# Kernel optimization log

Measured on AMD Instinct MI355X. Metric: run time of the kernel, lower is better.

Reference implementation:

```python
import jax, jax.numpy as jnp
import numpy as np

HID = 512
N_INT = 131072
N_INIT = 32768


def setup_inputs() -> dict:
    key = jax.random.key(0)
    ks = jax.random.split(key, 12)
    d = {}
    d["xt_int"] = jax.random.uniform(ks[0], (N_INT, 2), dtype=jnp.float32)
    d["f"] = 0.1 * jax.random.normal(ks[1], (N_INT, 1), dtype=jnp.float32)
    d["xt_init"] = jax.random.uniform(ks[2], (N_INIT, 2), dtype=jnp.float32)
    d["g"] = 0.1 * jax.random.normal(ks[3], (N_INIT, 1), dtype=jnp.float32)
    d["g_deriv"] = 0.1 * jax.random.normal(ks[4], (N_INIT, 1), dtype=jnp.float32)
    # tanh MLP 2 -> 512 -> 512 -> 512 -> 512 -> 1, Glorot-ish init
    def w(k, fi, fo):
        return jax.random.normal(k, (fi, fo), dtype=jnp.float32) * jnp.sqrt(2.0 / (fi + fo)).astype(jnp.float32)
    d["W0"] = w(ks[5], 2, HID);   d["b0"] = jnp.zeros((HID,), jnp.float32)
    d["W1"] = w(ks[6], HID, HID); d["b1"] = jnp.zeros((HID,), jnp.float32)
    d["W2"] = w(ks[7], HID, HID); d["b2"] = jnp.zeros((HID,), jnp.float32)
    d["W3"] = w(ks[8], HID, HID); d["b3"] = jnp.zeros((HID,), jnp.float32)
    d["W4"] = w(ks[9], HID, 1);   d["b4"] = jnp.zeros((1,), jnp.float32)
    d["c"] = jnp.ones((1,), jnp.float32)  # wave speed parameter
    return d


def _mlp(xt, Ws, bs):
    h = xt
    for W, b in zip(Ws[:-1], bs[:-1]):
        h = jnp.tanh(h @ W + b)
    return h @ Ws[-1] + bs[-1]  # [N, 1]


def reference(xt_int, f, xt_init, g, g_deriv, W0, b0, W1, b1, W2, b2, W3, b3, W4, b4, c):
    Ws = [W0, W1, W2, W3, W4]
    bs = [b0, b1, b2, b3, b4]
    net = lambda xt: _mlp(xt, Ws, bs)

    # --- initial-condition loss: 0.5/n * ||u(x,0) - g||^2
    n_init = xt_init.shape[0]
    pred_init = net(xt_init)
    loss_init = 0.5 / n_init * jnp.sum((pred_init - g) ** 2)

    # --- Neumann initial loss: u_t via forward-mode (tangent e_t = (0,1))
    e_t_init = jnp.broadcast_to(jnp.array([0.0, 1.0], jnp.float32), xt_init.shape)
    u_t_init = jax.jvp(net, (xt_init,), (e_t_init,))[1]
    loss_init_deriv = 0.5 / n_init * jnp.sum((u_t_init - g_deriv) ** 2)

    # --- PDE residual: u_tt - c^2 * u_xx via nested JVPs (batched, big GEMMs)
    n_int = xt_int.shape[0]

    def dir_deriv(v):
        # first directional derivative of net along constant direction v
        def d1(z):
            return jax.jvp(net, (z,), (jnp.broadcast_to(v, z.shape),))[1]
        return d1

    e_t = jnp.array([0.0, 1.0], jnp.float32)
    e_x = jnp.array([1.0, 0.0], jnp.float32)
    u_tt = jax.jvp(dir_deriv(e_t), (xt_int,), (jnp.broadcast_to(e_t, xt_int.shape),))[1]
    u_xx = jax.jvp(dir_deriv(e_x), (xt_int,), (jnp.broadcast_to(e_x, xt_int.shape),))[1]
    pred_f = u_tt - (c ** 2) * u_xx  # [N_INT, 1]
    loss_f = 0.5 / n_int * jnp.sum((pred_f - f) ** 2)

    return (loss_init, loss_init_deriv, loss_f)
```

## Files before the change

kernel.cpp:

```cpp
#include <hip/hip_runtime.h>
#include <hip/hip_bf16.h>
#include <cstdint>
#include <cstddef>

#define HID 512
#define N_INT 131072
#define N_INIT 32768
#define WT1 ((size_t)HID * HID)

typedef __attribute__((ext_vector_type(8))) short short8_t;
typedef __attribute__((ext_vector_type(4))) short short4_t;
typedef __attribute__((ext_vector_type(4))) float floatx4;

__device__ __forceinline__ float bf2f(unsigned short u) {
  return __uint_as_float(((unsigned)u) << 16);
}
__device__ __forceinline__ unsigned short f2bf_rne(float x) {
  unsigned u = __float_as_uint(x);
  unsigned r = u + 0x7FFF + ((u >> 16) & 1);
  return (unsigned short)(r >> 16);
}

__device__ __forceinline__ unsigned pack_pair(float a, float b) {
  unsigned h;
  asm("v_cvt_pk_bf16_f32 %0, %1, %2" : "=v"(h) : "v"(a), "v"(b));
  return h;
}

__device__ __forceinline__ float tanh_fast(float a) {
  const float e = __expf(2.f * a);
  return 1.f - __fdividef(2.f, e + 1.f);
}

__global__ __launch_bounds__(512) void wpack(
    const float* __restrict__ W, unsigned short* __restrict__ Wf)
{
  int n = blockIdx.x;
  int k = threadIdx.x;
  float w = W[(size_t)k * HID + n];
  size_t o = ((((size_t)(n >> 4) * 16 + (k >> 5)) * 64
               + ((k >> 3) & 3) * 16 + (n & 15)) << 3) + (k & 7);
  Wf[o] = f2bf_rne(w);
}

template <int NS>
__global__ __launch_bounds__(512) void fused_mlp(
    const float* __restrict__ xt,
    const float* __restrict__ W0, const float* __restrict__ b0,
    const unsigned short* __restrict__ Wf,
    const float* __restrict__ b1, const float* __restrict__ b2,
    const float* __restrict__ b3,
    const float* __restrict__ W4, const float* __restrict__ b4,
    const float* __restrict__ cc,
    const float* __restrict__ t0,
    const float* __restrict__ t1,
    float* __restrict__ out, float scale)
{
  __shared__ unsigned short Ald[NS * 8192];

  const int tid = threadIdx.x;
  const long rowbase = (long)blockIdx.x * 16;
  const int lane = tid & 63;
  const int wv = tid >> 6;
  const int row = lane & 15;
  const int kq = lane >> 4;

  {
    const int r0 = tid & 15;
    const int cg = tid >> 4;
    const long gr = rowbase + r0;
    const float x = xt[gr * 2 + 0];
    const float tv = xt[gr * 2 + 1];
#pragma unroll
    for (int sc = 0; sc < 2; ++sc) {
      const int j0 = cg * 16 + sc * 8;
      float v[NS][8];
#pragma unroll
      for (int jj = 0; jj < 8; ++jj) {
        const float wx = W0[j0 + jj];
        const float wt = W0[HID + j0 + jj];
        const float a = fmaf(x, wx, fmaf(tv, wt, b0[j0 + jj]));
        const float y = tanh_fast(a);
        const float d = 1.f - y * y;
        v[0][jj] = y;
        v[1][jj] = d * wt;
        if (NS == 5) {
          v[2][jj] = -2.f * y * d * wt * wt;
          v[3][jj] = d * wx;
          v[4][jj] = -2.f * y * d * wx * wx;
        }
      }
      const int di = ((j0 >> 5) << 9) + ((((j0 >> 3) & 3) * 16 + r0) << 3);
#pragma unroll
      for (int p = 0; p < NS; ++p) {
        union { unsigned u[4]; short8_t s8; } H;
#pragma unroll
        for (int q = 0; q < 4; ++q)
          H.u[q] = pack_pair(v[p][2 * q], v[p][2 * q + 1]);
        *(short8_t*)&Ald[p * 8192 + di] = H.s8;
      }
    }
  }
  __syncthreads();

  for (int L = 0; L < 3; ++L) {
    const unsigned short* __restrict__ WH = Wf + (size_t)L * WT1;

    floatx4 acc[NS][4];
#pragma unroll
    for (int s = 0; s < NS; ++s)
#pragma unroll
      for (int cf = 0; cf < 4; ++cf)
#pragma unroll
        for (int e = 0; e < 4; ++e) acc[s][cf][e] = 0.f;

#pragma unroll 4
    for (int t = 0; t < 16; ++t) {
      short8_t ah[NS], bhv[4];
#pragma unroll
      for (int cf = 0; cf < 4; ++cf) {
        const size_t bo = (((size_t)((wv * 4 + cf) * 16 + t)) << 9) + (lane << 3);
        bhv[cf] = *(const short8_t*)(WH + bo);
      }
#pragma unroll
      for (int s = 0; s < NS; ++s)
        ah[s] = *(const short8_t*)&Ald[s * 8192 + (lane << 3) + (t << 9)];
      __builtin_amdgcn_s_setprio(1);
#pragma unroll
      for (int s = 0; s < NS; ++s)
#pragma unroll
        for (int cf = 0; cf < 4; ++cf)
          acc[s][cf] = __builtin_amdgcn_mfma_f32_16x16x32_bf16(bhv[cf], ah[s], acc[s][cf], 0, 0, 0);
      __builtin_amdgcn_s_setprio(0);
    }
    __syncthreads();

    if (L < 2) {
      const float* __restrict__ bias = (L == 0) ? b1 : b2;
#pragma unroll
      for (int cf = 0; cf < 4; ++cf) {
        const int n = (wv << 6) + (cf << 4) + (kq << 2);
        const float4 bv4 = *(const float4*)(bias + n);
        const float bvv[4] = {bv4.x, bv4.y, bv4.z, bv4.w};
        float v[NS][4];
#pragma unroll
        for (int j = 0; j < 4; ++j) {
          const float a0 = acc[0][cf][j] + bvv[j];
          const float y = tanh_fast(a0);
          const float d = 1.f - y * y;
          const float a1 = acc[1][cf][j];
          const float o1 = d * a1;
          v[0][j] = y;
          v[1][j] = o1;
          if (NS == 5) {
            const float a2 = acc[2][cf][j];
            const float a3 = acc[3][cf][j];
            const float a4 = acc[4][cf][j];
            v[2][j] = fmaf(-2.f * y * a1, o1, d * a2);
            v[3][j] = d * a3;
            v[4][j] = fmaf(-2.f * y * v[3][j], a3, d * a4);
          }
        }
        const int di = ((n >> 5) << 9) + ((((n >> 3) & 3) * 16 + row) << 3) + (n & 7);
#pragma unroll
        for (int p = 0; p < NS; ++p) {
          union { unsigned u[2]; short4_t s4; } H;
          H.u[0] = pack_pair(v[p][0], v[p][1]);
          H.u[1] = pack_pair(v[p][2], v[p][3]);
          *(short4_t*)&Ald[p * 8192 + di] = H.s4;
        }
      }
      __syncthreads();
    } else {
      float s0 = 0.f, s1 = 0.f;
#pragma unroll
      for (int cf = 0; cf < 4; ++cf) {
        const int n = (wv << 6) + (cf << 4) + (kq << 2);
        const float4 bv4 = *(const float4*)(b3 + n);
        const float4 w44 = *(const float4*)(W4 + n);
        const float bvv[4] = {bv4.x, bv4.y, bv4.z, bv4.w};
        const float wvv[4] = {w44.x, w44.y, w44.z, w44.w};
#pragma unroll
        for (int j = 0; j < 4; ++j) {
          const float a0 = acc[0][cf][j] + bvv[j];
          const float y = tanh_fast(a0);
          const float d = 1.f - y * y;
          const float a1 = acc[1][cf][j];
          const float o1 = d * a1;
          if (NS == 5) {
            const float a2 = acc[2][cf][j];
            const float a3 = acc[3][cf][j];
            const float a4 = acc[4][cf][j];
            const float o2 = fmaf(-2.f * y * a1, o1, d * a2);
            const float o3 = d * a3;
            const float o4 = fmaf(-2.f * y * o3, a3, d * a4);
            s0 = fmaf(o2, wvv[j], s0);
            s1 = fmaf(o4, wvv[j], s1);
          } else {
            s0 = fmaf(y, wvv[j], s0);
            s1 = fmaf(o1, wvv[j], s1);
          }
        }
      }
      s0 += __shfl_xor(s0, 16); s0 += __shfl_xor(s0, 32);
      s1 += __shfl_xor(s1, 16); s1 += __shfl_xor(s1, 32);
      float* scr = (float*)&Ald[0];
      if (lane < 16) {
        scr[(wv << 4) + lane] = s0;
        scr[128 + (wv << 4) + lane] = s1;
      }
      __syncthreads();
      if (tid < 16) {
        float q0 = 0.f, q1 = 0.f;
#pragma unroll
        for (int w = 0; w < 8; ++w) {
          q0 += scr[(w << 4) + tid];
          q1 += scr[128 + (w << 4) + tid];
        }
        if (NS == 5) {
          const float c0 = cc[0];
          const float pred = q0 - c0 * c0 * q1;
          const float r = pred - t0[rowbase + tid];
          float v = r * r;
#pragma unroll
          for (int off = 1; off < 16; off <<= 1) v += __shfl_xor(v, off);
          if (tid == 0) atomicAdd(out + 2, scale * v);
        } else {
          const float r0 = q0 + b4[0] - t0[rowbase + tid];
          const float r1 = q1 - t1[rowbase + tid];
          float v0 = r0 * r0, v1 = r1 * r1;
#pragma unroll
          for (int off = 1; off < 16; off <<= 1) {
            v0 += __shfl_xor(v0, off);
            v1 += __shfl_xor(v1, off);
          }
          if (tid == 0) {
            atomicAdd(out + 0, scale * v0);
            atomicAdd(out + 1, scale * v1);
          }
        }
      }
    }
  }
}

extern "C" void kernel_launch(void* const* d_in, const int* in_sizes, int n_in,
                              void* d_out, int out_size, void* d_ws, size_t ws_size,
                              hipStream_t stream)
{
  const float* xt_int  = (const float*)d_in[0];
  const float* f       = (const float*)d_in[1];
  const float* xt_init = (const float*)d_in[2];
  const float* g       = (const float*)d_in[3];
  const float* gd      = (const float*)d_in[4];
  const float* W0 = (const float*)d_in[5];
  const float* b0 = (const float*)d_in[6];
  const float* W1 = (const float*)d_in[7];
  const float* b1 = (const float*)d_in[8];
  const float* W2 = (const float*)d_in[9];
  const float* b2 = (const float*)d_in[10];
  const float* W3 = (const float*)d_in[11];
  const float* b3 = (const float*)d_in[12];
  const float* W4 = (const float*)d_in[13];
  const float* b4 = (const float*)d_in[14];
  const float* c  = (const float*)d_in[15];
  float* out = (float*)d_out;

  hipMemsetAsync(out, 0, 3 * sizeof(float), stream);

  unsigned short* Wt = (unsigned short*)d_ws;

  wpack<<<HID, HID, 0, stream>>>(W1, Wt + 0 * WT1);
  wpack<<<HID, HID, 0, stream>>>(W2, Wt + 1 * WT1);
  wpack<<<HID, HID, 0, stream>>>(W3, Wt + 2 * WT1);

  const float sc_f = 0.5f / (float)N_INT;
  const float sc_i = 0.5f / (float)N_INIT;

  fused_mlp<5><<<N_INT / 16, 512, 0, stream>>>(
      xt_int, W0, b0, Wt, b1, b2, b3, W4, b4, c, f, nullptr, out, sc_f);
  fused_mlp<2><<<N_INIT / 16, 512, 0, stream>>>(
      xt_init, W0, b0, Wt, b1, b2, b3, W4, b4, nullptr, g, gd, out, sc_i);
}
```

Baseline: 1.117 ms.

## Process 32 rows per block to halve weight fetches per row

Each block now handles two 16-row M tiles instead of one, so every weight fragment loaded from global memory feeds twice as many MFMAs. The goal is to halve weight traffic per sample, which dominates because each block streams all three 512x512 layers. In exchange, LDS use doubles (160 KB for NS=5) and accumulator registers double (NS*2*4 floatx4), which risks lower occupancy or spills. The grid shrinks by half.

```diff
diff --git a/kernel.cpp b/kernel.cpp
--- a/kernel.cpp
+++ b/kernel.cpp
@@ -56,24 +56,26 @@
     const float* __restrict__ t1,
     float* __restrict__ out, float scale)
 {
-  __shared__ unsigned short Ald[NS * 8192];
+  __shared__ unsigned short Ald[NS * 16384];
 
   const int tid = threadIdx.x;
-  const long rowbase = (long)blockIdx.x * 16;
+  const long rowbase = (long)blockIdx.x * 32;
   const int lane = tid & 63;
   const int wv = tid >> 6;
   const int row = lane & 15;
   const int kq = lane >> 4;
 
   {
-    const int r0 = tid & 15;
-    const int cg = tid >> 4;
+    const int r0 = tid & 31;
+    const int cg = tid >> 5;
     const long gr = rowbase + r0;
     const float x = xt[gr * 2 + 0];
     const float tv = xt[gr * 2 + 1];
-#pragma unroll
-    for (int sc = 0; sc < 2; ++sc) {
-      const int j0 = cg * 16 + sc * 8;
+    const int mtw = r0 >> 4;
+    const int rr = r0 & 15;
+#pragma unroll
+    for (int sc = 0; sc < 4; ++sc) {
+      const int j0 = cg * 32 + sc * 8;
       float v[NS][8];
 #pragma unroll
       for (int jj = 0; jj < 8; ++jj) {
@@ -90,47 +92,56 @@
           v[4][jj] = -2.f * y * d * wx * wx;
         }
       }
-      const int di = ((j0 >> 5) << 9) + ((((j0 >> 3) & 3) * 16 + r0) << 3);
+      const int di = (mtw << 13) + ((j0 >> 5) << 9)
+                   + ((((j0 >> 3) & 3) * 16 + rr) << 3);
 #pragma unroll
       for (int p = 0; p < NS; ++p) {
         union { unsigned u[4]; short8_t s8; } H;
 #pragma unroll
         for (int q = 0; q < 4; ++q)
           H.u[q] = pack_pair(v[p][2 * q], v[p][2 * q + 1]);
-        *(short8_t*)&Ald[p * 8192 + di] = H.s8;
+        *(short8_t*)&Ald[p * 16384 + di] = H.s8;
       }
     }
   }
   __syncthreads();
 
   for (int L = 0; L < 3; ++L) {
-    const unsigned short* __restrict__ WH = Wf + (size_t)L * WT1;
-
-    floatx4 acc[NS][4];
+    const unsigned short* __restrict__ bbase =
+        Wf + (size_t)L * WT1 + ((size_t)(wv * 4) << 13) + (lane << 3);
+
+    floatx4 acc[NS][2][4];
 #pragma unroll
     for (int s = 0; s < NS; ++s)
 #pragma unroll
-      for (int cf = 0; cf < 4; ++cf)
-#pragma unroll
-        for (int e = 0; e < 4; ++e) acc[s][cf][e] = 0.f;
+      for (int mt = 0; mt < 2; ++mt)
+#pragma unroll
+        for (int cf = 0; cf < 4; ++cf)
+#pragma unroll
+          for (int e = 0; e < 4; ++e) acc[s][mt][cf][e] = 0.f;
 
 #pragma unroll 4
     for (int t = 0; t < 16; ++t) {
-      short8_t ah[NS], bhv[4];
-#pragma unroll
-      for (int cf = 0; cf < 4; ++cf) {
-        const size_t bo = (((size_t)((wv * 4 + cf) * 16 + t)) << 9) + (lane << 3);
-        bhv[cf] = *(const short8_t*)(WH + bo);
-      }
+      short8_t bhv[4];
+#pragma unroll
+      for (int cf = 0; cf < 4; ++cf)
+        bhv[cf] = *(const short8_t*)(bbase + cf * 8192 + (t << 9));
+      short8_t ah[NS][2];
 #pragma unroll
       for (int s = 0; s < NS; ++s)
-        ah[s] = *(const short8_t*)&Ald[s * 8192 + (lane << 3) + (t << 9)];
+#pragma unroll
+        for (int mt = 0; mt < 2; ++mt)
+          ah[s][mt] = *(const short8_t*)&Ald[s * 16384 + (mt << 13)
+                                            + (lane << 3) + (t << 9)];
       __builtin_amdgcn_s_setprio(1);
 #pragma unroll
       for (int s = 0; s < NS; ++s)
 #pragma unroll
-        for (int cf = 0; cf < 4; ++cf)
-          acc[s][cf] = __builtin_amdgcn_mfma_f32_16x16x32_bf16(bhv[cf], ah[s], acc[s][cf], 0, 0, 0);
+        for (int mt = 0; mt < 2; ++mt)
+#pragma unroll
+          for (int cf = 0; cf < 4; ++cf)
+            acc[s][mt][cf] = __builtin_amdgcn_mfma_f32_16x16x32_bf16(
+                bhv[cf], ah[s][mt], acc[s][mt][cf], 0, 0, 0);
       __builtin_amdgcn_s_setprio(0);
     }
     __syncthreads();
@@ -138,84 +149,97 @@
     if (L < 2) {
       const float* __restrict__ bias = (L == 0) ? b1 : b2;
 #pragma unroll
-      for (int cf = 0; cf < 4; ++cf) {
-        const int n = (wv << 6) + (cf << 4) + (kq << 2);
-        const float4 bv4 = *(const float4*)(bias + n);
-        const float bvv[4] = {bv4.x, bv4.y, bv4.z, bv4.w};
-        float v[NS][4];
-#pragma unroll
-        for (int j = 0; j < 4; ++j) {
-          const float a0 = acc[0][cf][j] + bvv[j];
-          const float y = tanh_fast(a0);
-          const float d = 1.f - y * y;
-          const float a1 = acc[1][cf][j];
-          const float o1 = d * a1;
-          v[0][j] = y;
-          v[1][j] = o1;
-          if (NS == 5) {
-            const float a2 = acc[2][cf][j];
-            const float a3 = acc[3][cf][j];
-            const float a4 = acc[4][cf][j];
-            v[2][j] = fmaf(-2.f * y * a1, o1, d * a2);
-            v[3][j] = d * a3;
-            v[4][j] = fmaf(-2.f * y * v[3][j], a3, d * a4);
-          }
-        }
-        const int di = ((n >> 5) << 9) + ((((n >> 3) & 3) * 16 + row) << 3) + (n & 7);
-#pragma unroll
-        for (int p = 0; p < NS; ++p) {
-          union { unsigned u[2]; short4_t s4; } H;
-          H.u[0] = pack_pair(v[p][0], v[p][1]);
-          H.u[1] = pack_pair(v[p][2], v[p][3]);
-          *(short4_t*)&Ald[p * 8192 + di] = H.s4;
+      for (int mt = 0; mt < 2; ++mt) {
+#pragma unroll
+        for (int cf = 0; cf < 4; ++cf) {
+          const int n = (wv << 6) + (cf << 4) + (kq << 2);
+          const float4 bv4 = *(const float4*)(bias + n);
+          const float bvv[4] = {bv4.x, bv4.y, bv4.z, bv4.w};
+          float v[NS][4];
+#pragma unroll
+          for (int j = 0; j < 4; ++j) {
+            const float a0 = acc[0][mt][cf][j] + bvv[j];
+            const float y = tanh_fast(a0);
+            const float d = 1.f - y * y;
+            const float a1 = acc[1][mt][cf][j];
+            const float o1 = d * a1;
+            v[0][j] = y;
+            v[1][j] = o1;
+            if (NS == 5) {
+              const float a2 = acc[2][mt][cf][j];
+              const float a3 = acc[3][mt][cf][j];
+              const float a4 = acc[4][mt][cf][j];
+              v[2][j] = fmaf(-2.f * y * a1, o1, d * a2);
+              v[3][j] = d * a3;
+              v[4][j] = fmaf(-2.f * y * v[3][j], a3, d * a4);
+            }
+          }
+          const int di = (mt << 13) + ((n >> 5) << 9)
+                       + ((((n >> 3) & 3) * 16 + row) << 3) + (n & 7);
+#pragma unroll
+          for (int p = 0; p < NS; ++p) {
+            union { unsigned u[2]; short4_t s4; } H;
+            H.u[0] = pack_pair(v[p][0], v[p][1]);
+            H.u[1] = pack_pair(v[p][2], v[p][3]);
+            *(short4_t*)&Ald[p * 16384 + di] = H.s4;
+          }
         }
       }
       __syncthreads();
     } else {
-      float s0 = 0.f, s1 = 0.f;
-#pragma unroll
-      for (int cf = 0; cf < 4; ++cf) {
-        const int n = (wv << 6) + (cf << 4) + (kq << 2);
-        const float4 bv4 = *(const float4*)(b3 + n);
-        const float4 w44 = *(const float4*)(W4 + n);
-        const float bvv[4] = {bv4.x, bv4.y, bv4.z, bv4.w};
-        const float wvv[4] = {w44.x, w44.y, w44.z, w44.w};
-#pragma unroll
-        for (int j = 0; j < 4; ++j) {
-          const float a0 = acc[0][cf][j] + bvv[j];
-          const float y = tanh_fast(a0);
-          const float d = 1.f - y * y;
-          const float a1 = acc[1][cf][j];
-          const float o1 = d * a1;
-          if (NS == 5) {
-            const float a2 = acc[2][cf][j];
-            const float a3 = acc[3][cf][j];
-            const float a4 = acc[4][cf][j];
-            const float o2 = fmaf(-2.f * y * a1, o1, d * a2);
-            const float o3 = d * a3;
-            const float o4 = fmaf(-2.f * y * o3, a3, d * a4);
-            s0 = fmaf(o2, wvv[j], s0);
-            s1 = fmaf(o4, wvv[j], s1);
-          } else {
-            s0 = fmaf(y, wvv[j], s0);
-            s1 = fmaf(o1, wvv[j], s1);
-          }
-        }
-      }
-      s0 += __shfl_xor(s0, 16); s0 += __shfl_xor(s0, 32);
-      s1 += __shfl_xor(s1, 16); s1 += __shfl_xor(s1, 32);
+      float s0[2] = {0.f, 0.f}, s1[2] = {0.f, 0.f};
+#pragma unroll
+      for (int mt = 0; mt < 2; ++mt) {
+#pragma unroll
+        for (int cf = 0; cf < 4; ++cf) {
+          const int n = (wv << 6) + (cf << 4) + (kq << 2);
+          const float4 bv4 = *(const float4*)(b3 + n);
+          const float4 w44 = *(const float4*)(W4 + n);
+          const float bvv[4] = {bv4.x, bv4.y, bv4.z, bv4.w};
+          const float wvv[4] = {w44.x, w44.y, w44.z, w44.w};
+#pragma unroll
+          for (int j = 0; j < 4; ++j) {
+            const float a0 = acc[0][mt][cf][j] + bvv[j];
+            const float y = tanh_fast(a0);
+            const float d = 1.f - y * y;
+            const float a1 = acc[1][mt][cf][j];
+            const float o1 = d * a1;
+            if (NS == 5) {
+              const float a2 = acc[2][mt][cf][j];
+              const float a3 = acc[3][mt][cf][j];
+              const float a4 = acc[4][mt][cf][j];
+              const float o2 = fmaf(-2.f * y * a1, o1, d * a2);
+              const float o3 = d * a3;
+              const float o4 = fmaf(-2.f * y * o3, a3, d * a4);
+              s0[mt] = fmaf(o2, wvv[j], s0[mt]);
+              s1[mt] = fmaf(o4, wvv[j], s1[mt]);
+            } else {
+              s0[mt] = fmaf(y, wvv[j], s0[mt]);
+              s1[mt] = fmaf(o1, wvv[j], s1[mt]);
+            }
+          }
+        }
+      }
+#pragma unroll
+      for (int mt = 0; mt < 2; ++mt) {
+        s0[mt] += __shfl_xor(s0[mt], 16); s0[mt] += __shfl_xor(s0[mt], 32);
+        s1[mt] += __shfl_xor(s1[mt], 16); s1[mt] += __shfl_xor(s1[mt], 32);
+      }
       float* scr = (float*)&Ald[0];
       if (lane < 16) {
-        scr[(wv << 4) + lane] = s0;
-        scr[128 + (wv << 4) + lane] = s1;
+#pragma unroll
+        for (int mt = 0; mt < 2; ++mt) {
+          scr[(wv << 5) + (mt << 4) + lane] = s0[mt];
+          scr[256 + (wv << 5) + (mt << 4) + lane] = s1[mt];
+        }
       }
       __syncthreads();
-      if (tid < 16) {
+      if (tid < 32) {
         float q0 = 0.f, q1 = 0.f;
 #pragma unroll
         for (int w = 0; w < 8; ++w) {
-          q0 += scr[(w << 4) + tid];
-          q1 += scr[128 + (w << 4) + tid];
+          q0 += scr[(w << 5) + tid];
+          q1 += scr[256 + (w << 5) + tid];
         }
         if (NS == 5) {
           const float c0 = cc[0];
@@ -223,14 +247,14 @@
           const float r = pred - t0[rowbase + tid];
           float v = r * r;
 #pragma unroll
-          for (int off = 1; off < 16; off <<= 1) v += __shfl_xor(v, off);
+          for (int off = 1; off < 32; off <<= 1) v += __shfl_xor(v, off);
           if (tid == 0) atomicAdd(out + 2, scale * v);
         } else {
           const float r0 = q0 + b4[0] - t0[rowbase + tid];
           const float r1 = q1 - t1[rowbase + tid];
           float v0 = r0 * r0, v1 = r1 * r1;
 #pragma unroll
-          for (int off = 1; off < 16; off <<= 1) {
+          for (int off = 1; off < 32; off <<= 1) {
             v0 += __shfl_xor(v0, off);
             v1 += __shfl_xor(v1, off);
           }
@@ -277,8 +301,8 @@
   const float sc_f = 0.5f / (float)N_INT;
   const float sc_i = 0.5f / (float)N_INIT;
 
-  fused_mlp<5><<<N_INT / 16, 512, 0, stream>>>(
+  fused_mlp<5><<<N_INT / 32, 512, 0, stream>>>(
       xt_int, W0, b0, Wt, b1, b2, b3, W4, b4, c, f, nullptr, out, sc_f);
-  fused_mlp<2><<<N_INIT / 16, 512, 0, stream>>>(
+  fused_mlp<2><<<N_INIT / 32, 512, 0, stream>>>(
       xt_init, W0, b0, Wt, b1, b2, b3, W4, b4, nullptr, g, gd, out, sc_i);
 }
```

After: 964.2 us. -13.7%, faster.
